# Kernel tuning notes

Measured on AMD Instinct MI355X. Metric: run time of the kernel, lower is better.

## Reference

```python
import jax, jax.numpy as jnp
import numpy as np

HEADS = 16

def split_heads(v, heads):
    # NOTE: faithful to the source: reshape [B,S,D] -> [B,S,h_dim,heads], then
    # transpose to [B,heads,S,h_dim]. This interleaves channels across heads
    # (different from the standard [B,S,heads,h_dim] split).
    B, S, D = v.shape
    hd = D // heads
    return v.reshape(B, S, hd, heads).transpose(0, 3, 1, 2)

def merge_heads(v):
    # [B,heads,S,h_dim] -> transpose [B,S,h_dim,heads] -> reshape [B,S,D]
    B, H, S, hd = v.shape
    return v.transpose(0, 2, 3, 1).reshape(B, S, H * hd)

def setup_inputs() -> dict:
    key = jax.random.key(0)
    ks = jax.random.split(key, 5)
    B, S, D = 2, 2048, 1024
    return {
        "x": jax.random.normal(ks[0], (B, S, D), dtype=jnp.float32),
        "qw": jax.random.normal(ks[1], (D, D), dtype=jnp.float32),
        "kw": jax.random.normal(ks[2], (D, D), dtype=jnp.float32),
        "vw": jax.random.normal(ks[3], (D, D), dtype=jnp.float32),
        "ow": jax.random.normal(ks[4], (D, D), dtype=jnp.float32),
    }

def reference(x, qw, kw, vw, ow):
    B, S, D = x.shape
    Q = split_heads(x @ qw, HEADS)  # [B,H,S,hd]
    K = split_heads(x @ kw, HEADS)
    V = split_heads(x @ vw, HEADS)
    # NOTE: scale is 1/sqrt(dim), NOT 1/sqrt(head_dim), as in the source.
    scale = 1.0 / jnp.sqrt(jnp.float32(D))
    score = jnp.einsum("bhqd,bhkd->bhqk", Q, K) * scale  # [B,H,S,S]
    causal = jnp.tril(jnp.ones((1, 1, S, S), dtype=score.dtype))
    score = score - 1e10 * (1.0 - causal)
    weights = jax.nn.softmax(score, axis=-1)
    attn = jnp.einsum("bhqk,bhkd->bhqd", weights, V)
    return merge_heads(attn) @ ow
```

## Files before the change

### kernel.cpp

```cpp
#include <hip/hip_runtime.h>


typedef __bf16 bf16x8 __attribute__((ext_vector_type(8)));
typedef float  f32x4  __attribute__((ext_vector_type(4)));

#define S_LEN  2048
#define DMODEL 1024
#define NHEADS 16
#define HDIM   64
#define LOG2E  1.44269504088896340736f

__device__ __forceinline__ void gll16(const __bf16* g, __bf16* l) {
    __builtin_amdgcn_global_load_lds(
        (const __attribute__((address_space(1))) unsigned int*)g,
        (__attribute__((address_space(3))) unsigned int*)l, 16, 0, 0);
}

__global__ __launch_bounds__(256) void prep_all(
    const float* __restrict__ x,
    const float* __restrict__ qw, const float* __restrict__ kw,
    const float* __restrict__ vw, const float* __restrict__ ow,
    __bf16* __restrict__ xhi, __bf16* __restrict__ xlo,
    __bf16* __restrict__ qwthi, __bf16* __restrict__ qwtlo,
    __bf16* __restrict__ kwthi, __bf16* __restrict__ kwtlo,
    __bf16* __restrict__ vwt,  __bf16* __restrict__ owt) {
    __shared__ float tile[32][33];
    int id = blockIdx.x;
    if (id < 4096) {
        int i = id * 256 + threadIdx.x;
        float4 v = ((const float4*)x)[i];
        __bf16 h0 = (__bf16)v.x, h1 = (__bf16)v.y, h2 = (__bf16)v.z, h3 = (__bf16)v.w;
        ushort4 hh, ll;
        hh.x = __builtin_bit_cast(unsigned short, h0);
        hh.y = __builtin_bit_cast(unsigned short, h1);
        hh.z = __builtin_bit_cast(unsigned short, h2);
        hh.w = __builtin_bit_cast(unsigned short, h3);
        ll.x = __builtin_bit_cast(unsigned short, (__bf16)(v.x - (float)h0));
        ll.y = __builtin_bit_cast(unsigned short, (__bf16)(v.y - (float)h1));
        ll.z = __builtin_bit_cast(unsigned short, (__bf16)(v.z - (float)h2));
        ll.w = __builtin_bit_cast(unsigned short, (__bf16)(v.w - (float)h3));
        ((ushort4*)xhi)[i] = hh;
        ((ushort4*)xlo)[i] = ll;
        return;
    }
    int rid = id - 4096;
    int z = rid >> 10;
    int bx = rid & 31, by = (rid >> 5) & 31;
    const float* w = (z == 0) ? qw : (z == 1) ? kw : (z == 2) ? vw : ow;
    int n0 = bx * 32, k0 = by * 32;
    int tx = threadIdx.x & 31, ty = threadIdx.x >> 5;
#pragma unroll
    for (int i = 0; i < 32; i += 8)
        tile[ty + i][tx] = w[(k0 + ty + i) * DMODEL + n0 + tx];
    __syncthreads();
#pragma unroll
    for (int i = 0; i < 32; i += 8) {
        float f = tile[tx][ty + i];
        int k = k0 + tx, n = n0 + ty + i;
        if (z <= 1) {
            __bf16 fh = (__bf16)f;
            __bf16 fl = (__bf16)(f - (float)fh);
            int c = (n & 15) * 64 + (n >> 4);
            if (z == 0) { qwthi[c * DMODEL + k] = fh; qwtlo[c * DMODEL + k] = fl; }
            else        { kwthi[c * DMODEL + k] = fh; kwtlo[c * DMODEL + k] = fl; }
        } else if (z == 2) {
            vwt[n * DMODEL + k] = (__bf16)f;
        } else {
            int ck = (k & 15) * 64 + (k >> 4);
            owt[n * DMODEL + ck] = (__bf16)f;
        }
    }
}

__global__ __launch_bounds__(256) void qkv_gemm(
    const __bf16* __restrict__ xhi, const __bf16* __restrict__ xlo,
    const __bf16* __restrict__ qwthi, const __bf16* __restrict__ qwtlo,
    const __bf16* __restrict__ kwthi, const __bf16* __restrict__ kwtlo,
    const __bf16* __restrict__ vwt,
    __bf16* __restrict__ Qhi, __bf16* __restrict__ Qlo,
    __bf16* __restrict__ Khi, __bf16* __restrict__ Klo,
    __bf16* __restrict__ Vt) {
    __shared__ __bf16 Ash[128][32], Asl[128][32], Bsh[128][32], Bsl[128][32];
    int mode = blockIdx.z;
    int tid  = threadIdx.x;
    int wave = tid >> 6, lane = tid & 63;
    int quad = lane >> 4, l15 = lane & 15;
    int wm = (wave >> 1) * 64, wn = (wave & 1) * 64;
    int grow = lane >> 2;
    int gcol = (((lane & 3) - ((lane >> 3) & 3)) & 3) * 8;
    int sA   = ((quad + (l15 >> 1)) & 3) * 8;
    const int K = DMODEL;

    if (mode < 2) {
        const __bf16* Bh = mode ? kwthi : qwthi;
        const __bf16* Bl = mode ? kwtlo : qwtlo;
        int m0 = blockIdx.y * 128, n0 = blockIdx.x * 128;
        f32x4 acc[4][4] = {};
        for (int k0 = 0; k0 < K; k0 += 32) {
            __syncthreads();
#pragma unroll
            for (int ps = 0; ps < 2; ps++) {
                int row = ps * 64 + wave * 16;
                gll16(&xhi[(m0 + row + grow) * K + k0 + gcol], &Ash[row][0]);
                gll16(&xlo[(m0 + row + grow) * K + k0 + gcol], &Asl[row][0]);
                gll16(&Bh [(n0 + row + grow) * K + k0 + gcol], &Bsh[row][0]);
                gll16(&Bl [(n0 + row + grow) * K + k0 + gcol], &Bsl[row][0]);
            }
            __syncthreads();
            bf16x8 ah[4], al[4], bh[4], bl[4];
#pragma unroll
            for (int mi = 0; mi < 4; mi++) {
                ah[mi] = *(const bf16x8*)&Ash[wm + mi * 16 + l15][sA];
                al[mi] = *(const bf16x8*)&Asl[wm + mi * 16 + l15][sA];
            }
#pragma unroll
            for (int ni = 0; ni < 4; ni++) {
                bh[ni] = *(const bf16x8*)&Bsh[wn + ni * 16 + l15][sA];
                bl[ni] = *(const bf16x8*)&Bsl[wn + ni * 16 + l15][sA];
            }
#pragma unroll
            for (int mi = 0; mi < 4; mi++)
#pragma unroll
                for (int ni = 0; ni < 4; ni++) {
                    acc[mi][ni] = __builtin_amdgcn_mfma_f32_16x16x32_bf16(ah[mi], bh[ni], acc[mi][ni], 0, 0, 0);
                    acc[mi][ni] = __builtin_amdgcn_mfma_f32_16x16x32_bf16(ah[mi], bl[ni], acc[mi][ni], 0, 0, 0);
                    acc[mi][ni] = __builtin_amdgcn_mfma_f32_16x16x32_bf16(al[mi], bh[ni], acc[mi][ni], 0, 0, 0);
                }
        }
        float oscale = mode ? 1.0f : 0.03125f * LOG2E;
        __bf16* Ohi = mode ? Khi : Qhi;
        __bf16* Olo = mode ? Klo : Qlo;
#pragma unroll
        for (int mi = 0; mi < 4; mi++)
#pragma unroll
            for (int ni = 0; ni < 4; ni++)
#pragma unroll
                for (int rg = 0; rg < 4; rg++) {
                    int m = m0 + wm + mi * 16 + quad * 4 + rg;
                    int n = n0 + wn + ni * 16 + l15;
                    float v = acc[mi][ni][rg] * oscale;
                    size_t idx = (size_t)m * DMODEL + n;
                    __bf16 vh = (__bf16)v;
                    Ohi[idx] = vh;
                    Olo[idx] = (__bf16)(v - (float)vh);
                }
    } else {
        int ch0 = blockIdx.x * 128, xm0 = blockIdx.y * 128;
        f32x4 acc[4][4] = {};
        for (int k0 = 0; k0 < K; k0 += 32) {
            __syncthreads();
#pragma unroll
            for (int ps = 0; ps < 2; ps++) {
                int row = ps * 64 + wave * 16;
                gll16(&vwt[(ch0 + row + grow) * K + k0 + gcol], &Ash[row][0]);
                gll16(&xhi[(xm0 + row + grow) * K + k0 + gcol], &Bsh[row][0]);
            }
            __syncthreads();
            bf16x8 af[4], bfr[4];
#pragma unroll
            for (int mi = 0; mi < 4; mi++)
                af[mi] = *(const bf16x8*)&Ash[wm + mi * 16 + l15][sA];
#pragma unroll
            for (int ni = 0; ni < 4; ni++)
                bfr[ni] = *(const bf16x8*)&Bsh[wn + ni * 16 + l15][sA];
#pragma unroll
            for (int mi = 0; mi < 4; mi++)
#pragma unroll
                for (int ni = 0; ni < 4; ni++)
                    acc[mi][ni] = __builtin_amdgcn_mfma_f32_16x16x32_bf16(
                        af[mi], bfr[ni], acc[mi][ni], 0, 0, 0);
        }
#pragma unroll
        for (int mi = 0; mi < 4; mi++)
#pragma unroll
            for (int ni = 0; ni < 4; ni++)
#pragma unroll
                for (int rg = 0; rg < 4; rg++) {
                    int ch = ch0 + wm + mi * 16 + quad * 4 + rg;
                    int xm = xm0 + wn + ni * 16 + l15;
                    int b = xm >> 11, s = xm & 2047;
                    int h = ch & 15,  d = ch >> 4;
                    Vt[((size_t)(b * NHEADS + h) * HDIM + d) * S_LEN + s] =
                        (__bf16)acc[mi][ni][rg];
                }
    }
}

__global__ __launch_bounds__(256) void out_gemm(const __bf16* __restrict__ A,
                                                const __bf16* __restrict__ Bt,
                                                float* __restrict__ out) {
    __shared__ __bf16 As[64][32];
    __shared__ __bf16 Bs[128][32];
    int tid  = threadIdx.x;
    int wave = tid >> 6, lane = tid & 63;
    int quad = lane >> 4, l15 = lane & 15;
    int m0 = blockIdx.y * 64, n0 = blockIdx.x * 128;
    int wm = (wave >> 1) * 32, wn = (wave & 1) * 64;
    int grow = lane >> 2;
    int gcol = (((lane & 3) - ((lane >> 3) & 3)) & 3) * 8;
    int sA   = ((quad + (l15 >> 1)) & 3) * 8;
    const int K = DMODEL;
    f32x4 acc[2][4] = {};

    for (int k0 = 0; k0 < K; k0 += 32) {
        __syncthreads();
        gll16(&A[(m0 + wave * 16 + grow) * K + k0 + gcol], &As[wave * 16][0]);
#pragma unroll
        for (int ps = 0; ps < 2; ps++) {
            int row = ps * 64 + wave * 16;
            gll16(&Bt[(n0 + row + grow) * K + k0 + gcol], &Bs[row][0]);
        }
        __syncthreads();
        bf16x8 af[2], bfr[4];
#pragma unroll
        for (int mi = 0; mi < 2; mi++)
            af[mi] = *(const bf16x8*)&As[wm + mi * 16 + l15][sA];
#pragma unroll
        for (int ni = 0; ni < 4; ni++)
            bfr[ni] = *(const bf16x8*)&Bs[wn + ni * 16 + l15][sA];
#pragma unroll
        for (int mi = 0; mi < 2; mi++)
#pragma unroll
            for (int ni = 0; ni < 4; ni++)
                acc[mi][ni] = __builtin_amdgcn_mfma_f32_16x16x32_bf16(
                    af[mi], bfr[ni], acc[mi][ni], 0, 0, 0);
    }

#pragma unroll
    for (int mi = 0; mi < 2; mi++)
#pragma unroll
        for (int ni = 0; ni < 4; ni++)
#pragma unroll
            for (int rg = 0; rg < 4; rg++) {
                int m = m0 + wm + mi * 16 + quad * 4 + rg;
                int n = n0 + wn + ni * 16 + l15;
                out[(size_t)m * DMODEL + n] = acc[mi][ni][rg];
            }
}

__global__ __launch_bounds__(256, 4) void flash_attn(const __bf16* __restrict__ Qhi,
                                                     const __bf16* __restrict__ Qlo,
                                                     const __bf16* __restrict__ Khi,
                                                     const __bf16* __restrict__ Klo,
                                                     const __bf16* __restrict__ Vt,
                                                     __bf16* __restrict__ attn) {
    int id  = blockIdx.x;
    int xcd = id & 7, r = id >> 3;
    int bh  = xcd + 8 * (r & 3);
    int t   = 31 - (r >> 2);
    int b = bh >> 4, h = bh & 15;
    const __bf16* Qh_hi = Qhi + (size_t)b * S_LEN * DMODEL + h * HDIM;
    const __bf16* Qh_lo = Qlo + (size_t)b * S_LEN * DMODEL + h * HDIM;
    const __bf16* Kh_hi = Khi + (size_t)b * S_LEN * DMODEL + h * HDIM;
    const __bf16* Kh_lo = Klo + (size_t)b * S_LEN * DMODEL + h * HDIM;
    const __bf16* Vh    = Vt  + (size_t)bh * HDIM * S_LEN;

    int tid = threadIdx.x, wave = tid >> 6, lane = tid & 63;
    int quad = lane >> 4, l15 = lane & 15;
    int iters = t + 1;

    __shared__ __bf16 KhF[8 * 64 * 8];
    __shared__ __bf16 KlF[8 * 64 * 8];
    __shared__ __bf16 VF [8 * 64 * 8];
    __shared__ __bf16 Ps[4][16][72];

    int c1  = tid >> 6, key = tid & 63;
    int inner = (c1 * 16 + (key & 15)) * 8;
    int rK    = (key >> 4);
    int kdst0 = rK * 512 + inner, kdst1 = (4 + rK) * 512 + inner;
    const __bf16* vrow = Vh + (size_t)key * S_LEN;

    int q0w = t * 64 + wave * 16;
    bf16x8 aqh0 = *(const bf16x8*)&Qh_hi[(size_t)(q0w + l15) * DMODEL + quad * 8];
    bf16x8 aqh1 = *(const bf16x8*)&Qh_hi[(size_t)(q0w + l15) * DMODEL + 32 + quad * 8];
    bf16x8 aql0 = *(const bf16x8*)&Qh_lo[(size_t)(q0w + l15) * DMODEL + quad * 8];
    bf16x8 aql1 = *(const bf16x8*)&Qh_lo[(size_t)(q0w + l15) * DMODEL + 32 + quad * 8];

    bf16x8 ones;
#pragma unroll
    for (int j = 0; j < 8; j++) ones[j] = (__bf16)1.0f;

    uint4 pk0, pk1, pl0, pl1, pv0, pv1;
    {
        const __bf16* sk = Kh_hi + (size_t)key * DMODEL;
        const __bf16* sl = Kh_lo + (size_t)key * DMODEL;
        pk0 = *(const uint4*)(sk + c1 * 8); pk1 = *(const uint4*)(sk + c1 * 8 + 32);
        pl0 = *(const uint4*)(sl + c1 * 8); pl1 = *(const uint4*)(sl + c1 * 8 + 32);
        pv0 = *(const uint4*)(vrow + c1 * 8); pv1 = *(const uint4*)(vrow + c1 * 8 + 32);
    }

    float m[4] = {-3e38f, -3e38f, -3e38f, -3e38f};
    f32x4 o[4] = {};
    f32x4 ol = {};
    int qrb = q0w + quad * 4;

    for (int i = 0; i < iters; i++) {
        int key0 = i * 64;
        bool diag = (i == iters - 1);

        __syncthreads();
        *(uint4*)&KhF[kdst0] = pk0;  *(uint4*)&KhF[kdst1] = pk1;
        *(uint4*)&KlF[kdst0] = pl0;  *(uint4*)&KlF[kdst1] = pl1;
        *(uint4*)&VF [kdst0] = pv0;  *(uint4*)&VF [kdst1] = pv1;
        __syncthreads();

        if (i + 1 < iters) {
            int key0n = (i + 1) * 64;
            const __bf16* sk = Kh_hi + (size_t)(key0n + key) * DMODEL;
            const __bf16* sl = Kh_lo + (size_t)(key0n + key) * DMODEL;
            pk0 = *(const uint4*)(sk + c1 * 8); pk1 = *(const uint4*)(sk + c1 * 8 + 32);
            pl0 = *(const uint4*)(sl + c1 * 8); pl1 = *(const uint4*)(sl + c1 * 8 + 32);
            pv0 = *(const uint4*)(vrow + key0n + c1 * 8);
            pv1 = *(const uint4*)(vrow + key0n + c1 * 8 + 32);
        }

        f32x4 sc[4] = {};
#pragma unroll
        for (int ni = 0; ni < 4; ni++) {
            bf16x8 kh0 = *(const bf16x8*)&KhF[(ni * 64 + lane) * 8];
            bf16x8 kh1 = *(const bf16x8*)&KhF[((4 + ni) * 64 + lane) * 8];
            bf16x8 kl0 = *(const bf16x8*)&KlF[(ni * 64 + lane) * 8];
            bf16x8 kl1 = *(const bf16x8*)&KlF[((4 + ni) * 64 + lane) * 8];
            sc[ni] = __builtin_amdgcn_mfma_f32_16x16x32_bf16(aqh0, kh0, sc[ni], 0, 0, 0);
            sc[ni] = __builtin_amdgcn_mfma_f32_16x16x32_bf16(aqh1, kh1, sc[ni], 0, 0, 0);
            sc[ni] = __builtin_amdgcn_mfma_f32_16x16x32_bf16(aqh0, kl0, sc[ni], 0, 0, 0);
            sc[ni] = __builtin_amdgcn_mfma_f32_16x16x32_bf16(aqh1, kl1, sc[ni], 0, 0, 0);
            sc[ni] = __builtin_amdgcn_mfma_f32_16x16x32_bf16(aql0, kh0, sc[ni], 0, 0, 0);
            sc[ni] = __builtin_amdgcn_mfma_f32_16x16x32_bf16(aql1, kh1, sc[ni], 0, 0, 0);
        }

        if (diag) {
#pragma unroll
            for (int ni = 0; ni < 4; ni++) {
                int keyi = key0 + ni * 16 + l15;
#pragma unroll
                for (int rg = 0; rg < 4; rg++)
                    if (keyi > qrb + rg) sc[ni][rg] = -1e30f;
            }
        }

#pragma unroll
        for (int rg = 0; rg < 4; rg++) {
            float mx = fmaxf(fmaxf(sc[0][rg], sc[1][rg]),
                             fmaxf(sc[2][rg], sc[3][rg]));
#pragma unroll
            for (int mm = 1; mm < 16; mm <<= 1)
                mx = fmaxf(mx, __shfl_xor(mx, mm, 64));
            float mnew  = fmaxf(m[rg], mx);
            float alpha = __builtin_amdgcn_exp2f(m[rg] - mnew);
            m[rg] = mnew;
#pragma unroll
            for (int ni = 0; ni < 4; ni++) {
                float px = __builtin_amdgcn_exp2f(sc[ni][rg] - mnew);
                Ps[wave][quad * 4 + rg][ni * 16 + l15] = (__bf16)px;
            }
            ol[rg] *= alpha;
#pragma unroll
            for (int ni = 0; ni < 4; ni++)
                o[ni][rg] *= alpha;
        }

#pragma unroll
        for (int step = 0; step < 2; step++) {
            bf16x8 ap = *(const bf16x8*)&Ps[wave][l15][step * 32 + quad * 8];
            ol = __builtin_amdgcn_mfma_f32_16x16x32_bf16(ap, ones, ol, 0, 0, 0);
#pragma unroll
            for (int ni = 0; ni < 4; ni++) {
                bf16x8 bv = *(const bf16x8*)&VF[((step * 4 + ni) * 64 + lane) * 8];
                o[ni] = __builtin_amdgcn_mfma_f32_16x16x32_bf16(ap, bv, o[ni], 0, 0, 0);
            }
        }
    }

#pragma unroll
    for (int rg = 0; rg < 4; rg++) {
        float inv = 1.0f / ol[rg];
        int q = q0w + quad * 4 + rg;
#pragma unroll
        for (int ni = 0; ni < 4; ni++) {
            attn[((size_t)b * S_LEN + q) * DMODEL + h * HDIM + ni * 16 + l15] =
                (__bf16)(o[ni][rg] * inv);
        }
    }
}

extern "C" void kernel_launch(void* const* d_in, const int* in_sizes, int n_in,
                              void* d_out, int out_size, void* d_ws, size_t ws_size,
                              hipStream_t stream) {
    const float* x  = (const float*)d_in[0];
    const float* qw = (const float*)d_in[1];
    const float* kw = (const float*)d_in[2];
    const float* vw = (const float*)d_in[3];
    const float* ow = (const float*)d_in[4];

    char* ws = (char*)d_ws;
    const size_t MB = 1024 * 1024;
    __bf16* xhi   = (__bf16*)(ws);
    __bf16* xlo   = (__bf16*)(ws + 8 * MB);
    __bf16* qwthi = (__bf16*)(ws + 16 * MB);
    __bf16* qwtlo = (__bf16*)(ws + 18 * MB);
    __bf16* kwthi = (__bf16*)(ws + 20 * MB);
    __bf16* kwtlo = (__bf16*)(ws + 22 * MB);
    __bf16* vwt   = (__bf16*)(ws + 24 * MB);
    __bf16* owt   = (__bf16*)(ws + 26 * MB);
    __bf16* Qhi_b = (__bf16*)(ws + 28 * MB);
    __bf16* Qlo_b = (__bf16*)(ws + 36 * MB);
    __bf16* Khi_b = (__bf16*)(ws + 44 * MB);
    __bf16* Klo_b = (__bf16*)(ws + 52 * MB);
    __bf16* Vtb   = (__bf16*)(ws + 60 * MB);
    __bf16* attnb = xlo;

    prep_all<<<8192, 256, 0, stream>>>(x, qw, kw, vw, ow,
                                       xhi, xlo, qwthi, qwtlo, kwthi, kwtlo,
                                       vwt, owt);

    qkv_gemm<<<dim3(8, 32, 3), 256, 0, stream>>>(
        xhi, xlo, qwthi, qwtlo, kwthi, kwtlo, vwt,
        Qhi_b, Qlo_b, Khi_b, Klo_b, Vtb);

    flash_attn<<<1024, 256, 0, stream>>>(Qhi_b, Qlo_b, Khi_b, Klo_b, Vtb, attnb);

    out_gemm<<<dim3(8, 64), 256, 0, stream>>>(attnb, owt, (float*)d_out);
}
```

Baseline: 248.0 us.

## Split long causal query tiles into two KV halves with a combine kernel

```diff
diff --git a/kernel.cpp b/kernel.cpp
--- a/kernel.cpp
+++ b/kernel.cpp
@@ -243,11 +243,31 @@
                                                      const __bf16* __restrict__ Khi,
                                                      const __bf16* __restrict__ Klo,
                                                      const __bf16* __restrict__ Vt,
-                                                     __bf16* __restrict__ attn) {
-    int id  = blockIdx.x;
-    int xcd = id & 7, r = id >> 3;
-    int bh  = xcd + 8 * (r & 3);
-    int t   = 31 - (r >> 2);
+                                                     __bf16* __restrict__ attn,
+                                                     float* __restrict__ po0,
+                                                     float* __restrict__ po1,
+                                                     float* __restrict__ pml) {
+    int id = blockIdx.x;
+    int bh, t, i0, i1, part;
+    bool split;
+    if (id < 1024) {
+        int xcd = id & 7, r = id >> 3;
+        bh = xcd + 8 * (r & 3);
+        int rr = r >> 2;
+        t = 31 - (rr >> 1);
+        part = rr & 1;
+        int h = (t + 1) >> 1;
+        i0 = part ? h : 0;
+        i1 = part ? (t + 1) : h;
+        split = true;
+    } else {
+        int id2 = id - 1024;
+        int xcd = id2 & 7, r = id2 >> 3;
+        bh = xcd + 8 * (r & 3);
+        t = 15 - (r >> 2);
+        part = 0; i0 = 0; i1 = t + 1;
+        split = false;
+    }
     int b = bh >> 4, h = bh & 15;
     const __bf16* Qh_hi = Qhi + (size_t)b * S_LEN * DMODEL + h * HDIM;
     const __bf16* Qh_lo = Qlo + (size_t)b * S_LEN * DMODEL + h * HDIM;
@@ -257,7 +277,6 @@
 
     int tid = threadIdx.x, wave = tid >> 6, lane = tid & 63;
     int quad = lane >> 4, l15 = lane & 15;
-    int iters = t + 1;
 
     __shared__ __bf16 KhF[8 * 64 * 8];
     __shared__ __bf16 KlF[8 * 64 * 8];
@@ -282,11 +301,12 @@
 
     uint4 pk0, pk1, pl0, pl1, pv0, pv1;
     {
-        const __bf16* sk = Kh_hi + (size_t)key * DMODEL;
-        const __bf16* sl = Kh_lo + (size_t)key * DMODEL;
+        const __bf16* sk = Kh_hi + (size_t)(i0 * 64 + key) * DMODEL;
+        const __bf16* sl = Kh_lo + (size_t)(i0 * 64 + key) * DMODEL;
         pk0 = *(const uint4*)(sk + c1 * 8); pk1 = *(const uint4*)(sk + c1 * 8 + 32);
         pl0 = *(const uint4*)(sl + c1 * 8); pl1 = *(const uint4*)(sl + c1 * 8 + 32);
-        pv0 = *(const uint4*)(vrow + c1 * 8); pv1 = *(const uint4*)(vrow + c1 * 8 + 32);
+        pv0 = *(const uint4*)(vrow + i0 * 64 + c1 * 8);
+        pv1 = *(const uint4*)(vrow + i0 * 64 + c1 * 8 + 32);
     }
 
     float m[4] = {-3e38f, -3e38f, -3e38f, -3e38f};
@@ -294,9 +314,9 @@
     f32x4 ol = {};
     int qrb = q0w + quad * 4;
 
-    for (int i = 0; i < iters; i++) {
+    for (int i = i0; i < i1; i++) {
         int key0 = i * 64;
-        bool diag = (i == iters - 1);
+        bool diag = (i == t);
 
         __syncthreads();
         *(uint4*)&KhF[kdst0] = pk0;  *(uint4*)&KhF[kdst1] = pk1;
@@ -304,7 +324,7 @@
         *(uint4*)&VF [kdst0] = pv0;  *(uint4*)&VF [kdst1] = pv1;
         __syncthreads();
 
-        if (i + 1 < iters) {
+        if (i + 1 < i1) {
             int key0n = (i + 1) * 64;
             const __bf16* sk = Kh_hi + (size_t)(key0n + key) * DMODEL;
             const __bf16* sl = Kh_lo + (size_t)(key0n + key) * DMODEL;
@@ -372,15 +392,62 @@
         }
     }
 
-#pragma unroll
-    for (int rg = 0; rg < 4; rg++) {
-        float inv = 1.0f / ol[rg];
-        int q = q0w + quad * 4 + rg;
-#pragma unroll
-        for (int ni = 0; ni < 4; ni++) {
-            attn[((size_t)b * S_LEN + q) * DMODEL + h * HDIM + ni * 16 + l15] =
-                (__bf16)(o[ni][rg] * inv);
-        }
+    if (!split) {
+#pragma unroll
+        for (int rg = 0; rg < 4; rg++) {
+            float inv = 1.0f / ol[rg];
+            int q = q0w + quad * 4 + rg;
+#pragma unroll
+            for (int ni = 0; ni < 4; ni++) {
+                attn[((size_t)b * S_LEN + q) * DMODEL + h * HDIM + ni * 16 + l15] =
+                    (__bf16)(o[ni][rg] * inv);
+            }
+        }
+    } else {
+        int pair = bh * 16 + (t - 16);
+        float* po = part ? po1 : po0;
+        float* pm = pml + ((size_t)part * 512 + pair) * 128;
+#pragma unroll
+        for (int rg = 0; rg < 4; rg++) {
+            int row = wave * 16 + quad * 4 + rg;
+            if (l15 == 0) { pm[row] = m[rg]; pm[64 + row] = ol[rg]; }
+#pragma unroll
+            for (int ni = 0; ni < 4; ni++)
+                po[((size_t)pair * 64 + row) * 64 + ni * 16 + l15] = o[ni][rg];
+        }
+    }
+}
+
+__global__ __launch_bounds__(256) void combine(const float* __restrict__ po0,
+                                               const float* __restrict__ po1,
+                                               const float* __restrict__ pml,
+                                               __bf16* __restrict__ attn) {
+    int pair = blockIdx.x;
+    int bh = pair >> 4, t = 16 + (pair & 15);
+    int b = bh >> 4, h = bh & 15;
+    int tid = threadIdx.x;
+    int row = tid >> 2, c = (tid & 3) * 16;
+
+    const float* m0p = pml + (size_t)pair * 128;
+    const float* m1p = pml + (size_t)512 * 128 + (size_t)pair * 128;
+    float m0 = m0p[row], l0 = m0p[64 + row];
+    float m1 = m1p[row], l1 = m1p[64 + row];
+    float mm = fmaxf(m0, m1);
+    float s0 = __builtin_amdgcn_exp2f(m0 - mm);
+    float s1 = __builtin_amdgcn_exp2f(m1 - mm);
+    float inv = 1.0f / (l0 * s0 + l1 * s1);
+
+    const float* r0 = po0 + ((size_t)pair * 64 + row) * 64 + c;
+    const float* r1 = po1 + ((size_t)pair * 64 + row) * 64 + c;
+    int q = t * 64 + row;
+    __bf16* dst = attn + ((size_t)b * S_LEN + q) * DMODEL + h * HDIM + c;
+#pragma unroll
+    for (int j = 0; j < 16; j += 4) {
+        f32x4 a  = *(const f32x4*)(r0 + j);
+        f32x4 bb = *(const f32x4*)(r1 + j);
+#pragma unroll
+        for (int e = 0; e < 4; e++)
+            dst[j + e] = (__bf16)((a[e] * s0 + bb[e] * s1) * inv);
     }
 }
 
@@ -409,6 +476,9 @@
     __bf16* Klo_b = (__bf16*)(ws + 52 * MB);
     __bf16* Vtb   = (__bf16*)(ws + 60 * MB);
     __bf16* attnb = xlo;
+    float* po0 = (float*)(ws);
+    float* po1 = (float*)(ws + 16 * MB);
+    float* pml = (float*)(ws + 24 * MB);
 
     prep_all<<<8192, 256, 0, stream>>>(x, qw, kw, vw, ow,
                                        xhi, xlo, qwthi, qwtlo, kwthi, kwtlo,
@@ -418,7 +488,10 @@
         xhi, xlo, qwthi, qwtlo, kwthi, kwtlo, vwt,
         Qhi_b, Qlo_b, Khi_b, Klo_b, Vtb);
 
-    flash_attn<<<1024, 256, 0, stream>>>(Qhi_b, Qlo_b, Khi_b, Klo_b, Vtb, attnb);
+    flash_attn<<<1536, 256, 0, stream>>>(Qhi_b, Qlo_b, Khi_b, Klo_b, Vtb, attnb,
+                                         po0, po1, pml);
+
+    combine<<<512, 256, 0, stream>>>(po0, po1, pml, attnb);
 
     out_gemm<<<dim3(8, 64), 256, 0, stream>>>(attnb, owt, (float*)d_out);
 }
```

Measured after the change: 251.0 us. About the same (+1.2%).

## Double flash-attention query tile to 128 rows per block for K/V reuse

Applied to the files above, without the earlier changes.

```diff
diff --git a/kernel.cpp b/kernel.cpp
--- a/kernel.cpp
+++ b/kernel.cpp
@@ -238,7 +238,7 @@
             }
 }
 
-__global__ __launch_bounds__(256, 4) void flash_attn(const __bf16* __restrict__ Qhi,
+__global__ __launch_bounds__(256, 2) void flash_attn(const __bf16* __restrict__ Qhi,
                                                      const __bf16* __restrict__ Qlo,
                                                      const __bf16* __restrict__ Khi,
                                                      const __bf16* __restrict__ Klo,
@@ -247,7 +247,8 @@
     int id  = blockIdx.x;
     int xcd = id & 7, r = id >> 3;
     int bh  = xcd + 8 * (r & 3);
-    int t   = 31 - (r >> 2);
+    int rr  = r >> 2;
+    int t   = (rr < 8) ? (15 - rr) : (rr - 8);
     int b = bh >> 4, h = bh & 15;
     const __bf16* Qh_hi = Qhi + (size_t)b * S_LEN * DMODEL + h * HDIM;
     const __bf16* Qh_lo = Qlo + (size_t)b * S_LEN * DMODEL + h * HDIM;
@@ -257,12 +258,12 @@
 
     int tid = threadIdx.x, wave = tid >> 6, lane = tid & 63;
     int quad = lane >> 4, l15 = lane & 15;
-    int iters = t + 1;
+    int iters = 2 * t + 2;
 
     __shared__ __bf16 KhF[8 * 64 * 8];
     __shared__ __bf16 KlF[8 * 64 * 8];
     __shared__ __bf16 VF [8 * 64 * 8];
-    __shared__ __bf16 Ps[4][16][72];
+    __shared__ __bf16 Ps[4][32][72];
 
     int c1  = tid >> 6, key = tid & 63;
     int inner = (c1 * 16 + (key & 15)) * 8;
@@ -270,11 +271,16 @@
     int kdst0 = rK * 512 + inner, kdst1 = (4 + rK) * 512 + inner;
     const __bf16* vrow = Vh + (size_t)key * S_LEN;
 
-    int q0w = t * 64 + wave * 16;
-    bf16x8 aqh0 = *(const bf16x8*)&Qh_hi[(size_t)(q0w + l15) * DMODEL + quad * 8];
-    bf16x8 aqh1 = *(const bf16x8*)&Qh_hi[(size_t)(q0w + l15) * DMODEL + 32 + quad * 8];
-    bf16x8 aql0 = *(const bf16x8*)&Qh_lo[(size_t)(q0w + l15) * DMODEL + quad * 8];
-    bf16x8 aql1 = *(const bf16x8*)&Qh_lo[(size_t)(q0w + l15) * DMODEL + 32 + quad * 8];
+    int qbase = t * 128 + wave * 32;
+    bf16x8 aqh0[2], aqh1[2], aql0[2], aql1[2];
+#pragma unroll
+    for (int qh = 0; qh < 2; qh++) {
+        size_t qr = (size_t)(qbase + qh * 16 + l15) * DMODEL;
+        aqh0[qh] = *(const bf16x8*)&Qh_hi[qr + quad * 8];
+        aqh1[qh] = *(const bf16x8*)&Qh_hi[qr + 32 + quad * 8];
+        aql0[qh] = *(const bf16x8*)&Qh_lo[qr + quad * 8];
+        aql1[qh] = *(const bf16x8*)&Qh_lo[qr + 32 + quad * 8];
+    }
 
     bf16x8 ones;
 #pragma unroll
@@ -289,14 +295,13 @@
         pv0 = *(const uint4*)(vrow + c1 * 8); pv1 = *(const uint4*)(vrow + c1 * 8 + 32);
     }
 
-    float m[4] = {-3e38f, -3e38f, -3e38f, -3e38f};
-    f32x4 o[4] = {};
-    f32x4 ol = {};
-    int qrb = q0w + quad * 4;
+    float m[2][4] = {{-3e38f, -3e38f, -3e38f, -3e38f},
+                     {-3e38f, -3e38f, -3e38f, -3e38f}};
+    f32x4 o[2][4] = {};
+    f32x4 ol[2] = {};
 
     for (int i = 0; i < iters; i++) {
         int key0 = i * 64;
-        bool diag = (i == iters - 1);
 
         __syncthreads();
         *(uint4*)&KhF[kdst0] = pk0;  *(uint4*)&KhF[kdst1] = pk1;
@@ -314,74 +319,91 @@
             pv1 = *(const uint4*)(vrow + key0n + c1 * 8 + 32);
         }
 
-        f32x4 sc[4] = {};
+        if (key0 > qbase + 31) continue;
+
+        f32x4 sc[2][4] = {};
 #pragma unroll
         for (int ni = 0; ni < 4; ni++) {
             bf16x8 kh0 = *(const bf16x8*)&KhF[(ni * 64 + lane) * 8];
             bf16x8 kh1 = *(const bf16x8*)&KhF[((4 + ni) * 64 + lane) * 8];
             bf16x8 kl0 = *(const bf16x8*)&KlF[(ni * 64 + lane) * 8];
             bf16x8 kl1 = *(const bf16x8*)&KlF[((4 + ni) * 64 + lane) * 8];
-            sc[ni] = __builtin_amdgcn_mfma_f32_16x16x32_bf16(aqh0, kh0, sc[ni], 0, 0, 0);
-            sc[ni] = __builtin_amdgcn_mfma_f32_16x16x32_bf16(aqh1, kh1, sc[ni], 0, 0, 0);
-            sc[ni] = __builtin_amdgcn_mfma_f32_16x16x32_bf16(aqh0, kl0, sc[ni], 0, 0, 0);
-            sc[ni] = __builtin_amdgcn_mfma_f32_16x16x32_bf16(aqh1, kl1, sc[ni], 0, 0, 0);
-            sc[ni] = __builtin_amdgcn_mfma_f32_16x16x32_bf16(aql0, kh0, sc[ni], 0, 0, 0);
-            sc[ni] = __builtin_amdgcn_mfma_f32_16x16x32_bf16(aql1, kh1, sc[ni], 0, 0, 0);
-        }
-
-        if (diag) {
-#pragma unroll
-            for (int ni = 0; ni < 4; ni++) {
-                int keyi = key0 + ni * 16 + l15;
-#pragma unroll
-                for (int rg = 0; rg < 4; rg++)
-                    if (keyi > qrb + rg) sc[ni][rg] = -1e30f;
-            }
-        }
-
-#pragma unroll
-        for (int rg = 0; rg < 4; rg++) {
-            float mx = fmaxf(fmaxf(sc[0][rg], sc[1][rg]),
-                             fmaxf(sc[2][rg], sc[3][rg]));
-#pragma unroll
-            for (int mm = 1; mm < 16; mm <<= 1)
-                mx = fmaxf(mx, __shfl_xor(mx, mm, 64));
-            float mnew  = fmaxf(m[rg], mx);
-            float alpha = __builtin_amdgcn_exp2f(m[rg] - mnew);
-            m[rg] = mnew;
-#pragma unroll
-            for (int ni = 0; ni < 4; ni++) {
-                float px = __builtin_amdgcn_exp2f(sc[ni][rg] - mnew);
-                Ps[wave][quad * 4 + rg][ni * 16 + l15] = (__bf16)px;
-            }
-            ol[rg] *= alpha;
-#pragma unroll
-            for (int ni = 0; ni < 4; ni++)
-                o[ni][rg] *= alpha;
+#pragma unroll
+            for (int qh = 0; qh < 2; qh++) {
+                sc[qh][ni] = __builtin_amdgcn_mfma_f32_16x16x32_bf16(aqh0[qh], kh0, sc[qh][ni], 0, 0, 0);
+                sc[qh][ni] = __builtin_amdgcn_mfma_f32_16x16x32_bf16(aqh1[qh], kh1, sc[qh][ni], 0, 0, 0);
+                sc[qh][ni] = __builtin_amdgcn_mfma_f32_16x16x32_bf16(aqh0[qh], kl0, sc[qh][ni], 0, 0, 0);
+                sc[qh][ni] = __builtin_amdgcn_mfma_f32_16x16x32_bf16(aqh1[qh], kl1, sc[qh][ni], 0, 0, 0);
+                sc[qh][ni] = __builtin_amdgcn_mfma_f32_16x16x32_bf16(aql0[qh], kh0, sc[qh][ni], 0, 0, 0);
+                sc[qh][ni] = __builtin_amdgcn_mfma_f32_16x16x32_bf16(aql1[qh], kh1, sc[qh][ni], 0, 0, 0);
+            }
+        }
+
+        if (i >= 2 * t) {
+#pragma unroll
+            for (int qh = 0; qh < 2; qh++) {
+                int qrb = qbase + qh * 16 + quad * 4;
+#pragma unroll
+                for (int ni = 0; ni < 4; ni++) {
+                    int keyi = key0 + ni * 16 + l15;
+#pragma unroll
+                    for (int rg = 0; rg < 4; rg++)
+                        if (keyi > qrb + rg) sc[qh][ni][rg] = -1e30f;
+                }
+            }
+        }
+
+#pragma unroll
+        for (int qh = 0; qh < 2; qh++) {
+#pragma unroll
+            for (int rg = 0; rg < 4; rg++) {
+                float mx = fmaxf(fmaxf(sc[qh][0][rg], sc[qh][1][rg]),
+                                 fmaxf(sc[qh][2][rg], sc[qh][3][rg]));
+#pragma unroll
+                for (int mm = 1; mm < 16; mm <<= 1)
+                    mx = fmaxf(mx, __shfl_xor(mx, mm, 64));
+                float mnew  = fmaxf(m[qh][rg], mx);
+                float alpha = __builtin_amdgcn_exp2f(m[qh][rg] - mnew);
+                m[qh][rg] = mnew;
+#pragma unroll
+                for (int ni = 0; ni < 4; ni++) {
+                    float px = __builtin_amdgcn_exp2f(sc[qh][ni][rg] - mnew);
+                    Ps[wave][qh * 16 + quad * 4 + rg][ni * 16 + l15] = (__bf16)px;
+                }
+                ol[qh][rg] *= alpha;
+#pragma unroll
+                for (int ni = 0; ni < 4; ni++)
+                    o[qh][ni][rg] *= alpha;
+            }
         }
 
 #pragma unroll
         for (int step = 0; step < 2; step++) {
-            bf16x8 ap = *(const bf16x8*)&Ps[wave][l15][step * 32 + quad * 8];
-            ol = __builtin_amdgcn_mfma_f32_16x16x32_bf16(ap, ones, ol, 0, 0, 0);
+            bf16x8 ap0 = *(const bf16x8*)&Ps[wave][l15][step * 32 + quad * 8];
+            bf16x8 ap1 = *(const bf16x8*)&Ps[wave][16 + l15][step * 32 + quad * 8];
+            ol[0] = __builtin_amdgcn_mfma_f32_16x16x32_bf16(ap0, ones, ol[0], 0, 0, 0);
+            ol[1] = __builtin_amdgcn_mfma_f32_16x16x32_bf16(ap1, ones, ol[1], 0, 0, 0);
 #pragma unroll
             for (int ni = 0; ni < 4; ni++) {
                 bf16x8 bv = *(const bf16x8*)&VF[((step * 4 + ni) * 64 + lane) * 8];
-                o[ni] = __builtin_amdgcn_mfma_f32_16x16x32_bf16(ap, bv, o[ni], 0, 0, 0);
-            }
-        }
-    }
-
-#pragma unroll
-    for (int rg = 0; rg < 4; rg++) {
-        float inv = 1.0f / ol[rg];
-        int q = q0w + quad * 4 + rg;
-#pragma unroll
-        for (int ni = 0; ni < 4; ni++) {
-            attn[((size_t)b * S_LEN + q) * DMODEL + h * HDIM + ni * 16 + l15] =
-                (__bf16)(o[ni][rg] * inv);
-        }
-    }
+                o[0][ni] = __builtin_amdgcn_mfma_f32_16x16x32_bf16(ap0, bv, o[0][ni], 0, 0, 0);
+                o[1][ni] = __builtin_amdgcn_mfma_f32_16x16x32_bf16(ap1, bv, o[1][ni], 0, 0, 0);
+            }
+        }
+    }
+
+#pragma unroll
+    for (int qh = 0; qh < 2; qh++)
+#pragma unroll
+        for (int rg = 0; rg < 4; rg++) {
+            float inv = 1.0f / ol[qh][rg];
+            int q = qbase + qh * 16 + quad * 4 + rg;
+#pragma unroll
+            for (int ni = 0; ni < 4; ni++) {
+                attn[((size_t)b * S_LEN + q) * DMODEL + h * HDIM + ni * 16 + l15] =
+                    (__bf16)(o[qh][ni][rg] * inv);
+            }
+        }
 }
 
 extern "C" void kernel_launch(void* const* d_in, const int* in_sizes, int n_in,
@@ -418,7 +440,7 @@
         xhi, xlo, qwthi, qwtlo, kwthi, kwtlo, vwt,
         Qhi_b, Qlo_b, Khi_b, Klo_b, Vtb);
 
-    flash_attn<<<1024, 256, 0, stream>>>(Qhi_b, Qlo_b, Khi_b, Klo_b, Vtb, attnb);
+    flash_attn<<<512, 256, 0, stream>>>(Qhi_b, Qlo_b, Khi_b, Klo_b, Vtb, attnb);
 
     out_gemm<<<dim3(8, 64), 256, 0, stream>>>(attnb, owt, (float*)d_out);
 }
```

Measured after the change: 259.9 us. +4.8%, slower.
